# Performance work log

Measured on AMD Instinct MI355X. Metric: run time of the kernel, lower is better.

## Reference

```python
import jax, jax.numpy as jnp
import numpy as np

B, S, D, H = 2, 2048, 1024, 16
DEPTH = D // H


def setup_inputs() -> dict:
    key = jax.random.key(0)
    ks = jax.random.split(key, 12)
    inp = {
        "q": jax.random.normal(ks[0], (B, S, D), jnp.float32),
        "k": jax.random.normal(ks[1], (B, S, D), jnp.float32),
        "v": jax.random.normal(ks[2], (B, S - 1, D), jnp.float32),
        # causal mask for the sliced (S-1, S-1) score grid: 1 where masked out
        "mask": jnp.broadcast_to(
            jnp.triu(jnp.ones((S - 1, S - 1), jnp.float32), k=1), (B, S - 1, S - 1)
        ),
        "Wq": jax.random.normal(ks[3], (D, D), jnp.float32) * 0.02,
        "bq": jnp.zeros((D,), jnp.float32),
        "Wk": jax.random.normal(ks[4], (D, D), jnp.float32) * 0.02,
        "bk": jnp.zeros((D,), jnp.float32),
        "Wv": jax.random.normal(ks[5], (D, D), jnp.float32) * 0.02,
        "bv": jnp.zeros((D,), jnp.float32),
        "Wo": jax.random.normal(ks[6], (D, D), jnp.float32) * 0.02,
        "bo": jnp.zeros((D,), jnp.float32),
    }
    return inp


def _split_heads(x):
    # (B, L, D) -> (B, H, L, depth)
    b, l, _ = x.shape
    return x.reshape(b, l, H, DEPTH).transpose(0, 2, 1, 3)


def reference(q, k, v, mask, Wq, bq, Wk, bk, Wv, bv, Wo, bo):
    qq = q @ Wq + bq            # q_layers[0]
    kk = k @ Wk + bk            # k_layers[0]
    vv = v @ Wv + bv            # wv
    qh, kh, vh = _split_heads(qq), _split_heads(kk), _split_heads(vv)
    # scores: (B, H, S, S) then sliced to (B, H, S-1, S-1) as in the source
    scores = jnp.einsum('bhqd,bhkd->bhqk', qh, kh)[:, :, 1:, :-1]
    scale = 1.0 / jnp.sqrt(jnp.asarray(DEPTH, jnp.float32))
    # original casts to fp64 here; JAX default x64-disabled => computed in fp32
    logits = scores * scale + mask[:, None, :, :] * (-1e9)
    att = jax.nn.softmax(logits, axis=-1)   # (B, H, S-1, S-1)
    ctx = jnp.einsum('bhqk,bhkd->bhqd', att, vh)  # v seq len is S-1
    ctx = ctx.transpose(0, 2, 1, 3).reshape(q.shape[0], -1, D)
    out = ctx @ Wo + bo
    return out, att
```

## Files before the change

### kernel.cpp

```cpp
#include <hip/hip_runtime.h>


typedef __attribute__((ext_vector_type(8))) short bf16x8;
typedef __attribute__((ext_vector_type(4))) float f32x4;

#define MFMA_BF16(A, B, C) __builtin_amdgcn_mfma_f32_16x16x32_bf16(A, B, C, 0, 0, 0)

__device__ __forceinline__ short f2bf(float x) {
    unsigned u = __float_as_uint(x);
    u = u + 0x7FFFu + ((u >> 16) & 1u);
    return (short)(u >> 16);
}
__device__ __forceinline__ float bf2f(short s) {
    return __uint_as_float(((unsigned)(unsigned short)s) << 16);
}
__device__ __forceinline__ int imin(int a, int b) { return a < b ? a : b; }

__device__ __forceinline__ float fexp2(float x) {
#if __has_builtin(__builtin_amdgcn_exp2f)
    return __builtin_amdgcn_exp2f(x);
#else
    return __expf(x * 0.69314718055994531f);
#endif
}

__device__ __forceinline__ void dma16(const short* g, short* l) {
    __builtin_amdgcn_global_load_lds(
        (const __attribute__((address_space(1))) unsigned int*)g,
        (__attribute__((address_space(3))) unsigned int*)l, 16, 0, 0);
}

__global__ __launch_bounds__(256) void transpose_split_kernel(
    const float* __restrict__ W, short* __restrict__ Thi, short* __restrict__ Tlo) {
    __shared__ float tile[32][33];
    const int tx = threadIdx.x & 31, ty = threadIdx.x >> 5;
    const int k0 = blockIdx.x * 32, n0 = blockIdx.y * 32;
#pragma unroll
    for (int p = 0; p < 4; ++p)
        tile[ty + p * 8][tx] = W[(size_t)(k0 + ty + p * 8) * 1024 + n0 + tx];
    __syncthreads();
#pragma unroll
    for (int p = 0; p < 4; ++p) {
        int n = n0 + ty + p * 8, k = k0 + tx;
        float x = tile[tx][ty + p * 8];
        short h = f2bf(x);
        Thi[(size_t)n * 1024 + k] = h;
        if (Tlo) Tlo[(size_t)n * 1024 + k] = f2bf(x - bf2f(h));
    }
}

__global__ __launch_bounds__(256) void split_kernel(
    const float* __restrict__ X, short* __restrict__ Hi, short* __restrict__ Lo, int n8) {
    int idx = blockIdx.x * 256 + threadIdx.x;
    if (idx >= n8) return;
    float4 x0 = *((const float4*)X + (size_t)idx * 2);
    float4 x1 = *((const float4*)X + (size_t)idx * 2 + 1);
    float xs[8] = {x0.x, x0.y, x0.z, x0.w, x1.x, x1.y, x1.z, x1.w};
    bf16x8 hv, lv;
#pragma unroll
    for (int e = 0; e < 8; ++e) {
        short h = f2bf(xs[e]);
        hv[e] = h;
        lv[e] = f2bf(xs[e] - bf2f(h));
    }
    *(bf16x8*)&Hi[(size_t)idx * 8] = hv;
    if (Lo) *(bf16x8*)&Lo[(size_t)idx * 8] = lv;
}

__global__ __launch_bounds__(256) void gemm_qkv(
    const short* __restrict__ Qhi, const short* __restrict__ Qlo,
    const short* __restrict__ Khi, const short* __restrict__ Klo,
    const short* __restrict__ Vbf,
    const short* __restrict__ Wqh, const short* __restrict__ Wql,
    const short* __restrict__ Wkh, const short* __restrict__ Wkl,
    const short* __restrict__ Wvh,
    const float* __restrict__ bq, const float* __restrict__ bk,
    const float* __restrict__ bv, float qscale,
    short* __restrict__ QQh, short* __restrict__ QQl,
    short* __restrict__ KKh, short* __restrict__ KKl,
    short* __restrict__ VVo) {
    __shared__ __align__(16) short Ah[512 * 8];
    __shared__ __align__(16) short Al[512 * 8];

    const int z = blockIdx.z;
    const bool split = (z < 2);
    const short* Ahg = (z == 0) ? Qhi : ((z == 1) ? Khi : Vbf);
    const short* Alg = (z == 0) ? Qlo : Klo;
    const short* Bhg = (z == 0) ? Wqh : ((z == 1) ? Wkh : Wvh);
    const short* Blg = (z == 0) ? Wql : Wkl;
    const float* bias = (z == 0) ? bq : ((z == 1) ? bk : bv);
    const float scale = (z == 0) ? qscale : 1.0f;
    const int M = (z == 2) ? 4094 : 4096;
    short* Chi = (z == 0) ? QQh : ((z == 1) ? KKh : VVo);
    short* Clo = (z == 0) ? QQl : KKl;

    const int tid = threadIdx.x;
    const int w = tid >> 6, lane = tid & 63;
    const int quad = lane >> 4, l16 = lane & 15;
    const int m0 = blockIdx.y * 128, n0 = blockIdx.x * 64;
    const int row0 = (w & 1) * 64, col0 = (w >> 1) * 32;

    f32x4 acc[4][2];
#pragma unroll
    for (int mi = 0; mi < 4; ++mi)
#pragma unroll
        for (int ni = 0; ni < 2; ++ni) acc[mi][ni] = (f32x4){0.f, 0.f, 0.f, 0.f};

    const int a_gr = imin(m0 + (tid & 127), M - 1);

    for (int k0 = 0; k0 < 1024; k0 += 32) {
        __syncthreads();
#pragma unroll
        for (int p = 0; p < 2; ++p) {
            int idx = p * 256 + tid;
            int c = idx >> 7;
            const size_t go = (size_t)a_gr * 1024 + k0 + c * 8;
            dma16(Ahg + go, &Ah[idx * 8]);
            if (split) dma16(Alg + go, &Al[idx * 8]);
        }
        bf16x8 bfh[2], bfl[2];
#pragma unroll
        for (int ni = 0; ni < 2; ++ni) {
            const size_t bo = (size_t)(n0 + col0 + ni * 16 + l16) * 1024 + k0 + quad * 8;
            bfh[ni] = *(const bf16x8*)&Bhg[bo];
            if (split) bfl[ni] = *(const bf16x8*)&Blg[bo];
        }
        __syncthreads();

        bf16x8 af[4], afl[4];
#pragma unroll
        for (int mi = 0; mi < 4; ++mi) {
            int r = row0 + mi * 16 + l16;
            af[mi] = *(const bf16x8*)&Ah[(quad * 128 + r) * 8];
            if (split) afl[mi] = *(const bf16x8*)&Al[(quad * 128 + r) * 8];
        }
#pragma unroll
        for (int mi = 0; mi < 4; ++mi)
#pragma unroll
            for (int ni = 0; ni < 2; ++ni) {
                acc[mi][ni] = MFMA_BF16(af[mi], bfh[ni], acc[mi][ni]);
                if (split) {
                    acc[mi][ni] = MFMA_BF16(af[mi], bfl[ni], acc[mi][ni]);
                    acc[mi][ni] = MFMA_BF16(afl[mi], bfh[ni], acc[mi][ni]);
                }
            }
    }

#pragma unroll
    for (int ni = 0; ni < 2; ++ni) {
        int col = n0 + col0 + ni * 16 + l16;
        float bv_ = bias[col];
#pragma unroll
        for (int mi = 0; mi < 4; ++mi) {
#pragma unroll
            for (int r = 0; r < 4; ++r) {
                int row = m0 + row0 + mi * 16 + quad * 4 + r;
                if (row < M) {
                    float c = (acc[mi][ni][r] + bv_) * scale;
                    size_t off = (size_t)row * 1024 + col;
                    short hsv = f2bf(c);
                    Chi[off] = hsv;
                    if (split) Clo[off] = f2bf(c - bf2f(hsv));
                }
            }
        }
    }
}

__global__ __launch_bounds__(256) void gemm_o(
    const short* __restrict__ Ahg, int M, const short* __restrict__ Bhg,
    const float* __restrict__ bias, float* __restrict__ Cf) {
    __shared__ __align__(16) short Ah[512 * 8];

    const int tid = threadIdx.x;
    const int w = tid >> 6, lane = tid & 63;
    const int quad = lane >> 4, l16 = lane & 15;
    const int m0 = blockIdx.y * 128, n0 = blockIdx.x * 64;
    const int row0 = (w & 1) * 64, col0 = (w >> 1) * 32;

    f32x4 acc[4][2];
#pragma unroll
    for (int mi = 0; mi < 4; ++mi)
#pragma unroll
        for (int ni = 0; ni < 2; ++ni) acc[mi][ni] = (f32x4){0.f, 0.f, 0.f, 0.f};

    const int a_gr = imin(m0 + (tid & 127), M - 1);

    for (int k0 = 0; k0 < 1024; k0 += 32) {
        __syncthreads();
#pragma unroll
        for (int p = 0; p < 2; ++p) {
            int idx = p * 256 + tid;
            int c = idx >> 7;
            dma16(Ahg + (size_t)a_gr * 1024 + k0 + c * 8, &Ah[idx * 8]);
        }
        bf16x8 bfh[2];
#pragma unroll
        for (int ni = 0; ni < 2; ++ni) {
            const size_t bo = (size_t)(n0 + col0 + ni * 16 + l16) * 1024 + k0 + quad * 8;
            bfh[ni] = *(const bf16x8*)&Bhg[bo];
        }
        __syncthreads();

        bf16x8 af[4];
#pragma unroll
        for (int mi = 0; mi < 4; ++mi)
            af[mi] = *(const bf16x8*)&Ah[(quad * 128 + row0 + mi * 16 + l16) * 8];
#pragma unroll
        for (int mi = 0; mi < 4; ++mi)
#pragma unroll
            for (int ni = 0; ni < 2; ++ni)
                acc[mi][ni] = MFMA_BF16(af[mi], bfh[ni], acc[mi][ni]);
    }

#pragma unroll
    for (int ni = 0; ni < 2; ++ni) {
        int col = n0 + col0 + ni * 16 + l16;
        float bv_ = bias[col];
#pragma unroll
        for (int mi = 0; mi < 4; ++mi)
#pragma unroll
            for (int r = 0; r < 4; ++r) {
                int row = m0 + row0 + mi * 16 + quad * 4 + r;
                if (row < M) Cf[(size_t)row * 1024 + col] = acc[mi][ni][r] + bv_;
            }
    }
}

__global__ __launch_bounds__(256) void transpose_v_kernel(
    const short* __restrict__ VV, short* __restrict__ VT) {
    __shared__ short t[64][72];
    const int tid = threadIdx.x;
    const int st = blockIdx.x & 31, bh = blockIdx.x >> 5;
    const int b = bh >> 4, h = bh & 15;
    const int s0 = st * 64;
    {
        int seq = s0 + (tid >> 2), d0 = (tid & 3) * 16;
        int seqc = imin(seq, 2046);
        const short* src = VV + ((size_t)(b * 2047 + seqc)) * 1024 + h * 64 + d0;
        bf16x8 v0 = *(const bf16x8*)src;
        bf16x8 v1 = *(const bf16x8*)(src + 8);
        bool ok = (seq <= 2046);
#pragma unroll
        for (int e = 0; e < 8; ++e) {
            t[d0 + e][tid >> 2] = ok ? v0[e] : (short)0;
            t[d0 + 8 + e][tid >> 2] = ok ? v1[e] : (short)0;
        }
    }
    __syncthreads();
    {
        int d = tid >> 2, sc2 = (tid & 3) * 16;
        bf16x8 o0, o1;
#pragma unroll
        for (int e = 0; e < 8; ++e) {
            o0[e] = t[d][sc2 + e];
            o1[e] = t[d][sc2 + 8 + e];
        }
        short* dst = VT + ((size_t)(bh * 64 + d)) * 2048 + s0 + sc2;
        *(bf16x8*)dst = o0;
        *(bf16x8*)(dst + 8) = o1;
    }
}

__global__ __launch_bounds__(512) void attn_kernel(
    const short* __restrict__ QQh, const short* __restrict__ QQl,
    const short* __restrict__ KKh, const short* __restrict__ KKl,
    const short* __restrict__ VT,
    float* __restrict__ att, short* __restrict__ CTX) {
    __shared__ __align__(16) short Kh[512 * 8];
    __shared__ __align__(16) short Kl[512 * 8];
    __shared__ __align__(16) short Vt[512 * 8];
    __shared__ __align__(16) short Ps[8][16 * 72];

    const int tid = threadIdx.x;
    const int w = tid >> 6, lane = tid & 63;
    const int quad = lane >> 4, l16 = lane & 15;
    const int bx = blockIdx.x;
    const int qt = 15 - (bx >> 5);
    const int bh = bx & 31;
    const int h = bh & 15, b = bh >> 4;
    const int i0 = qt * 128;

    const int i_frag = i0 + w * 16 + l16;
    const int qrow = imin(i_frag + 1, 2047);
    const size_t qoff = ((size_t)(b * 2048 + qrow)) * 1024 + h * 64;
    const bf16x8 qh0 = *(const bf16x8*)&QQh[qoff + 0 + quad * 8];
    const bf16x8 qh1 = *(const bf16x8*)&QQh[qoff + 32 + quad * 8];
    const bf16x8 ql0 = *(const bf16x8*)&QQl[qoff + 0 + quad * 8];
    const bf16x8 ql1 = *(const bf16x8*)&QQl[qoff + 32 + quad * 8];

    const int i_max = imin(i0 + 127, 2046);
    const int jt_max = i_max >> 6;
    const int wave_imax = imin(i0 + w * 16 + 15, 2046);
    const int rowbase = i0 + w * 16 + quad * 4;

    const int dk = tid & 63;
    const int dc = tid >> 6;

    float lsum[4] = {0.f, 0.f, 0.f, 0.f};

    auto stA = [&](int jt, short* dst) {
        dma16(KKh + ((size_t)(b * 2048 + jt * 64 + dk)) * 1024 + h * 64 + dc * 8,
              &dst[tid * 8]);
    };
    stA(0, Kh);
    __syncthreads();
    int cur = 0;
    for (int jt = 0; jt <= jt_max; ++jt) {
        if (jt < jt_max) stA(jt + 1, cur ? Kh : Kl);
        if (jt * 64 <= wave_imax) {
            const short* Kc = cur ? Kl : Kh;
#pragma unroll
            for (int s = 0; s < 4; ++s) {
                f32x4 sc = (f32x4){0.f, 0.f, 0.f, 0.f};
#pragma unroll
                for (int c = 0; c < 2; ++c) {
                    bf16x8 kh = *(const bf16x8*)&Kc[((c * 4 + quad) * 64 + s * 16 + l16) * 8];
                    sc = MFMA_BF16(c ? qh1 : qh0, kh, sc);
                    sc = MFMA_BF16(c ? ql1 : ql0, kh, sc);
                }
                int j = jt * 64 + s * 16 + l16;
#pragma unroll
                for (int r = 0; r < 4; ++r) {
                    int i = rowbase + r;
                    if (j <= i && i <= 2046) lsum[r] += fexp2(sc[r]);
                }
            }
        }
        __syncthreads();
        cur ^= 1;
    }
#pragma unroll
    for (int m = 1; m < 16; m <<= 1) {
#pragma unroll
        for (int r = 0; r < 4; ++r) lsum[r] += __shfl_xor(lsum[r], m, 64);
    }
    float linv[4];
#pragma unroll
    for (int r = 0; r < 4; ++r) linv[r] = 1.0f / lsum[r];

    f32x4 cacc[4];
#pragma unroll
    for (int t = 0; t < 4; ++t) cacc[t] = (f32x4){0.f, 0.f, 0.f, 0.f};

    for (int jt = 0; jt <= jt_max; ++jt) {
        const int j0 = jt * 64;
        __syncthreads();
        {
            const size_t ko = ((size_t)(b * 2048 + j0 + dk)) * 1024 + h * 64 + dc * 8;
            dma16(KKh + ko, &Kh[tid * 8]);
            dma16(KKl + ko, &Kl[tid * 8]);
            dma16(VT + ((size_t)(bh * 64 + dk)) * 2048 + j0 + dc * 8, &Vt[tid * 8]);
        }
        __syncthreads();
        if (j0 <= wave_imax) {
#pragma unroll
            for (int s = 0; s < 4; ++s) {
                f32x4 sc = (f32x4){0.f, 0.f, 0.f, 0.f};
#pragma unroll
                for (int c = 0; c < 2; ++c) {
                    const int ci = ((c * 4 + quad) * 64 + s * 16 + l16) * 8;
                    bf16x8 kh = *(const bf16x8*)&Kh[ci];
                    bf16x8 kl = *(const bf16x8*)&Kl[ci];
                    bf16x8 ah = c ? qh1 : qh0;
                    bf16x8 al = c ? ql1 : ql0;
                    sc = MFMA_BF16(ah, kh, sc);
                    sc = MFMA_BF16(ah, kl, sc);
                    sc = MFMA_BF16(al, kh, sc);
                }
                int j = j0 + s * 16 + l16;
#pragma unroll
                for (int r = 0; r < 4; ++r) {
                    int i = rowbase + r;
                    bool valid = (j <= i) && (i <= 2046);
                    float p = valid ? fexp2(sc[r]) * linv[r] : 0.0f;
                    if (i <= 2046 && j <= 2046)
                        att[((size_t)bh * 2047 + i) * 2047 + j] = p;
                    Ps[w][(quad * 4 + r) * 72 + s * 16 + l16] = f2bf(p);
                }
            }
#pragma unroll
            for (int c = 0; c < 2; ++c) {
                bf16x8 pa = *(const bf16x8*)&Ps[w][l16 * 72 + c * 32 + quad * 8];
#pragma unroll
                for (int t = 0; t < 4; ++t) {
                    bf16x8 vb = *(const bf16x8*)&Vt[((c * 4 + quad) * 64 + t * 16 + l16) * 8];
                    cacc[t] = MFMA_BF16(pa, vb, cacc[t]);
                }
            }
        } else {
#pragma unroll
            for (int s = 0; s < 4; ++s) {
                int j = j0 + s * 16 + l16;
#pragma unroll
                for (int r = 0; r < 4; ++r) {
                    int i = rowbase + r;
                    if (i <= 2046 && j <= 2046)
                        att[((size_t)bh * 2047 + i) * 2047 + j] = 0.0f;
                }
            }
        }
    }

#pragma unroll
    for (int t = 0; t < 4; ++t) {
#pragma unroll
        for (int r = 0; r < 4; ++r) {
            int i = rowbase + r;
            if (i <= 2046)
                CTX[((size_t)(b * 2047 + i)) * 1024 + h * 64 + t * 16 + l16] = f2bf(cacc[t][r]);
        }
    }

    const int js = (jt_max + 1) * 64;
    if (js < 2047) {
        const float4 z4 = {0.f, 0.f, 0.f, 0.f};
        for (int i = i0; i <= i_max; ++i) {
            const size_t base = (size_t)(bh * 2047 + i) * 2047;
            float* rowp = att + base;
            int aligned = js + (int)((4 - ((base + js) & 3)) & 3);
            if (aligned > 2047) aligned = 2047;
            for (int c = js + tid; c < aligned; c += 512) rowp[c] = 0.0f;
            int nv = (2047 - aligned) >> 2;
            for (int q = tid; q < nv; q += 512)
                *(float4*)(rowp + aligned + q * 4) = z4;
            for (int c = aligned + nv * 4 + tid; c < 2047; c += 512) rowp[c] = 0.0f;
        }
    }
}

extern "C" void kernel_launch(void* const* d_in, const int* in_sizes, int n_in,
                              void* d_out, int out_size, void* d_ws, size_t ws_size,
                              hipStream_t stream) {
    (void)in_sizes; (void)n_in; (void)out_size; (void)ws_size;
    const float* q  = (const float*)d_in[0];
    const float* k  = (const float*)d_in[1];
    const float* v  = (const float*)d_in[2];
    const float* Wq = (const float*)d_in[4];
    const float* bq = (const float*)d_in[5];
    const float* Wk = (const float*)d_in[6];
    const float* bk = (const float*)d_in[7];
    const float* Wv = (const float*)d_in[8];
    const float* bv = (const float*)d_in[9];
    const float* Wo = (const float*)d_in[10];
    const float* bo = (const float*)d_in[11];

    float* out = (float*)d_out;
    float* att = out + (size_t)2 * 2047 * 1024;

    char* ws = (char*)d_ws;
    size_t off = 0;
    auto alloc = [&](size_t bytes) -> void* {
        void* p = ws + off;
        off += (bytes + 255) & ~(size_t)255;
        return p;
    };
    short* Wqt_h = (short*)alloc((size_t)1024 * 1024 * 2);
    short* Wqt_l = (short*)alloc((size_t)1024 * 1024 * 2);
    short* Wkt_h = (short*)alloc((size_t)1024 * 1024 * 2);
    short* Wkt_l = (short*)alloc((size_t)1024 * 1024 * 2);
    short* Wvt_h = (short*)alloc((size_t)1024 * 1024 * 2);
    short* Wot_h = (short*)alloc((size_t)1024 * 1024 * 2);
    short* Qhi = (short*)alloc((size_t)4096 * 1024 * 2);
    short* Qlo = (short*)alloc((size_t)4096 * 1024 * 2);
    short* Khi = (short*)alloc((size_t)4096 * 1024 * 2);
    short* Klo = (short*)alloc((size_t)4096 * 1024 * 2);
    short* Vbf = (short*)alloc((size_t)4096 * 1024 * 2);
    short* QQh = (short*)alloc((size_t)4096 * 1024 * 2);
    short* QQl = (short*)alloc((size_t)4096 * 1024 * 2);
    short* KKh = (short*)alloc((size_t)4096 * 1024 * 2);
    short* KKl = (short*)alloc((size_t)4096 * 1024 * 2);
    short* VV  = (short*)alloc((size_t)4096 * 1024 * 2);
    short* VT  = (short*)alloc((size_t)2048 * 2048 * 2 * 2);
    short* CTX = (short*)alloc((size_t)4096 * 1024 * 2);

    dim3 tgrid(32, 32);
    transpose_split_kernel<<<tgrid, 256, 0, stream>>>(Wq, Wqt_h, Wqt_l);
    transpose_split_kernel<<<tgrid, 256, 0, stream>>>(Wk, Wkt_h, Wkt_l);
    transpose_split_kernel<<<tgrid, 256, 0, stream>>>(Wv, Wvt_h, nullptr);
    transpose_split_kernel<<<tgrid, 256, 0, stream>>>(Wo, Wot_h, nullptr);

    split_kernel<<<2048, 256, 0, stream>>>(q, Qhi, Qlo, 4096 * 1024 / 8);
    split_kernel<<<2048, 256, 0, stream>>>(k, Khi, Klo, 4096 * 1024 / 8);
    split_kernel<<<2047, 256, 0, stream>>>(v, Vbf, nullptr, 4094 * 1024 / 8);

    const float qscale = 0.125f * 1.44269504088896341f;
    gemm_qkv<<<dim3(16, 32, 3), 256, 0, stream>>>(
        Qhi, Qlo, Khi, Klo, Vbf, Wqt_h, Wqt_l, Wkt_h, Wkt_l, Wvt_h,
        bq, bk, bv, qscale, QQh, QQl, KKh, KKl, VV);

    transpose_v_kernel<<<dim3(32 * 32), 256, 0, stream>>>(VV, VT);

    attn_kernel<<<dim3(16 * 32), 512, 0, stream>>>(QQh, QQl, KKh, KKl, VT, att, CTX);

    gemm_o<<<dim3(16, 32), 256, 0, stream>>>(CTX, 4094, Wot_h, bo, out);
}
```

Before: 1.002 ms.

## Widen GEMM tiles to 128x128 with LDS-staged B, merge prep kernel launches

```diff
diff --git a/kernel.cpp b/kernel.cpp
--- a/kernel.cpp
+++ b/kernel.cpp
@@ -30,8 +30,17 @@
         (__attribute__((address_space(3))) unsigned int*)l, 16, 0, 0);
 }
 
-__global__ __launch_bounds__(256) void transpose_split_kernel(
-    const float* __restrict__ W, short* __restrict__ Thi, short* __restrict__ Tlo) {
+__global__ __launch_bounds__(256) void transpose_split4(
+    const float* __restrict__ Wq, const float* __restrict__ Wk,
+    const float* __restrict__ Wv, const float* __restrict__ Wo,
+    short* __restrict__ Tqh, short* __restrict__ Tql,
+    short* __restrict__ Tkh, short* __restrict__ Tkl,
+    short* __restrict__ Tvh, short* __restrict__ Toh) {
+    const int z = blockIdx.z;
+    const float* W = (z == 0) ? Wq : (z == 1) ? Wk : (z == 2) ? Wv : Wo;
+    short* Thi = (z == 0) ? Tqh : (z == 1) ? Tkh : (z == 2) ? Tvh : Toh;
+    short* Tlo = (z == 0) ? Tql : (z == 1) ? Tkl : nullptr;
+
     __shared__ float tile[32][33];
     const int tx = threadIdx.x & 31, ty = threadIdx.x >> 5;
     const int k0 = blockIdx.x * 32, n0 = blockIdx.y * 32;
@@ -49,8 +58,18 @@
     }
 }
 
-__global__ __launch_bounds__(256) void split_kernel(
-    const float* __restrict__ X, short* __restrict__ Hi, short* __restrict__ Lo, int n8) {
+__global__ __launch_bounds__(256) void split3(
+    const float* __restrict__ q, const float* __restrict__ k,
+    const float* __restrict__ v,
+    short* __restrict__ Qhi, short* __restrict__ Qlo,
+    short* __restrict__ Khi, short* __restrict__ Klo,
+    short* __restrict__ Vbf) {
+    const int z = blockIdx.z;
+    const float* X = (z == 0) ? q : (z == 1) ? k : v;
+    short* Hi = (z == 0) ? Qhi : (z == 1) ? Khi : Vbf;
+    short* Lo = (z == 0) ? Qlo : (z == 1) ? Klo : nullptr;
+    const int n8 = (z == 2) ? (4094 * 1024 / 8) : (4096 * 1024 / 8);
+
     int idx = blockIdx.x * 256 + threadIdx.x;
     if (idx >= n8) return;
     float4 x0 = *((const float4*)X + (size_t)idx * 2);
@@ -81,6 +100,8 @@
     short* __restrict__ VVo) {
     __shared__ __align__(16) short Ah[512 * 8];
     __shared__ __align__(16) short Al[512 * 8];
+    __shared__ __align__(16) short Bh[512 * 8];
+    __shared__ __align__(16) short Bl[512 * 8];
 
     const int z = blockIdx.z;
     const bool split = (z < 2);
@@ -97,68 +118,72 @@
     const int tid = threadIdx.x;
     const int w = tid >> 6, lane = tid & 63;
     const int quad = lane >> 4, l16 = lane & 15;
-    const int m0 = blockIdx.y * 128, n0 = blockIdx.x * 64;
-    const int row0 = (w & 1) * 64, col0 = (w >> 1) * 32;
-
-    f32x4 acc[4][2];
+    const int m0 = blockIdx.y * 128, n0 = blockIdx.x * 128;
+    const int wr = (w & 1) * 64, wc = (w >> 1) * 64;
+
+    f32x4 acc[4][4];
 #pragma unroll
     for (int mi = 0; mi < 4; ++mi)
 #pragma unroll
-        for (int ni = 0; ni < 2; ++ni) acc[mi][ni] = (f32x4){0.f, 0.f, 0.f, 0.f};
+        for (int ni = 0; ni < 4; ++ni) acc[mi][ni] = (f32x4){0.f, 0.f, 0.f, 0.f};
 
     const int a_gr = imin(m0 + (tid & 127), M - 1);
+    const int b_gr = n0 + (tid & 127);
 
     for (int k0 = 0; k0 < 1024; k0 += 32) {
         __syncthreads();
 #pragma unroll
         for (int p = 0; p < 2; ++p) {
-            int idx = p * 256 + tid;
-            int c = idx >> 7;
-            const size_t go = (size_t)a_gr * 1024 + k0 + c * 8;
-            dma16(Ahg + go, &Ah[idx * 8]);
-            if (split) dma16(Alg + go, &Al[idx * 8]);
-        }
-        bf16x8 bfh[2], bfl[2];
-#pragma unroll
-        for (int ni = 0; ni < 2; ++ni) {
-            const size_t bo = (size_t)(n0 + col0 + ni * 16 + l16) * 1024 + k0 + quad * 8;
-            bfh[ni] = *(const bf16x8*)&Bhg[bo];
-            if (split) bfl[ni] = *(const bf16x8*)&Blg[bo];
+            const int idx = p * 256 + tid;
+            const size_t ga = (size_t)a_gr * 1024 + k0 + (idx >> 7) * 8;
+            const size_t gb = (size_t)b_gr * 1024 + k0 + (idx >> 7) * 8;
+            dma16(Ahg + ga, &Ah[idx * 8]);
+            dma16(Bhg + gb, &Bh[idx * 8]);
+            if (split) {
+                dma16(Alg + ga, &Al[idx * 8]);
+                dma16(Blg + gb, &Bl[idx * 8]);
+            }
         }
         __syncthreads();
 
         bf16x8 af[4], afl[4];
 #pragma unroll
         for (int mi = 0; mi < 4; ++mi) {
-            int r = row0 + mi * 16 + l16;
+            const int r = wr + mi * 16 + l16;
             af[mi] = *(const bf16x8*)&Ah[(quad * 128 + r) * 8];
             if (split) afl[mi] = *(const bf16x8*)&Al[(quad * 128 + r) * 8];
         }
 #pragma unroll
-        for (int mi = 0; mi < 4; ++mi)
-#pragma unroll
-            for (int ni = 0; ni < 2; ++ni) {
-                acc[mi][ni] = MFMA_BF16(af[mi], bfh[ni], acc[mi][ni]);
-                if (split) {
-                    acc[mi][ni] = MFMA_BF16(af[mi], bfl[ni], acc[mi][ni]);
-                    acc[mi][ni] = MFMA_BF16(afl[mi], bfh[ni], acc[mi][ni]);
-                }
-            }
-    }
-
-#pragma unroll
-    for (int ni = 0; ni < 2; ++ni) {
-        int col = n0 + col0 + ni * 16 + l16;
-        float bv_ = bias[col];
+        for (int ni = 0; ni < 4; ++ni) {
+            const int cdx = wc + ni * 16 + l16;
+            const bf16x8 bfh = *(const bf16x8*)&Bh[(quad * 128 + cdx) * 8];
+#pragma unroll
+            for (int mi = 0; mi < 4; ++mi)
+                acc[mi][ni] = MFMA_BF16(af[mi], bfh, acc[mi][ni]);
+            if (split) {
+                const bf16x8 bfl = *(const bf16x8*)&Bl[(quad * 128 + cdx) * 8];
+#pragma unroll
+                for (int mi = 0; mi < 4; ++mi) {
+                    acc[mi][ni] = MFMA_BF16(af[mi], bfl, acc[mi][ni]);
+                    acc[mi][ni] = MFMA_BF16(afl[mi], bfh, acc[mi][ni]);
+                }
+            }
+        }
+    }
+
+#pragma unroll
+    for (int ni = 0; ni < 4; ++ni) {
+        const int col = n0 + wc + ni * 16 + l16;
+        const float bv_ = bias[col];
 #pragma unroll
         for (int mi = 0; mi < 4; ++mi) {
 #pragma unroll
             for (int r = 0; r < 4; ++r) {
-                int row = m0 + row0 + mi * 16 + quad * 4 + r;
+                const int row = m0 + wr + mi * 16 + quad * 4 + r;
                 if (row < M) {
-                    float c = (acc[mi][ni][r] + bv_) * scale;
-                    size_t off = (size_t)row * 1024 + col;
-                    short hsv = f2bf(c);
+                    const float c = (acc[mi][ni][r] + bv_) * scale;
+                    const size_t off = (size_t)row * 1024 + col;
+                    const short hsv = f2bf(c);
                     Chi[off] = hsv;
                     if (split) Clo[off] = f2bf(c - bf2f(hsv));
                 }
@@ -171,57 +196,55 @@
     const short* __restrict__ Ahg, int M, const short* __restrict__ Bhg,
     const float* __restrict__ bias, float* __restrict__ Cf) {
     __shared__ __align__(16) short Ah[512 * 8];
+    __shared__ __align__(16) short Bh[512 * 8];
 
     const int tid = threadIdx.x;
     const int w = tid >> 6, lane = tid & 63;
     const int quad = lane >> 4, l16 = lane & 15;
-    const int m0 = blockIdx.y * 128, n0 = blockIdx.x * 64;
-    const int row0 = (w & 1) * 64, col0 = (w >> 1) * 32;
-
-    f32x4 acc[4][2];
+    const int m0 = blockIdx.y * 128, n0 = blockIdx.x * 128;
+    const int wr = (w & 1) * 64, wc = (w >> 1) * 64;
+
+    f32x4 acc[4][4];
 #pragma unroll
     for (int mi = 0; mi < 4; ++mi)
 #pragma unroll
-        for (int ni = 0; ni < 2; ++ni) acc[mi][ni] = (f32x4){0.f, 0.f, 0.f, 0.f};
+        for (int ni = 0; ni < 4; ++ni) acc[mi][ni] = (f32x4){0.f, 0.f, 0.f, 0.f};
 
     const int a_gr = imin(m0 + (tid & 127), M - 1);
+    const int b_gr = n0 + (tid & 127);
 
     for (int k0 = 0; k0 < 1024; k0 += 32) {
         __syncthreads();
 #pragma unroll
         for (int p = 0; p < 2; ++p) {
-            int idx = p * 256 + tid;
-            int c = idx >> 7;
-            dma16(Ahg + (size_t)a_gr * 1024 + k0 + c * 8, &Ah[idx * 8]);
-        }
-        bf16x8 bfh[2];
-#pragma unroll
-        for (int ni = 0; ni < 2; ++ni) {
-            const size_t bo = (size_t)(n0 + col0 + ni * 16 + l16) * 1024 + k0 + quad * 8;
-            bfh[ni] = *(const bf16x8*)&Bhg[bo];
+            const int idx = p * 256 + tid;
+            dma16(Ahg + (size_t)a_gr * 1024 + k0 + (idx >> 7) * 8, &Ah[idx * 8]);
+            dma16(Bhg + (size_t)b_gr * 1024 + k0 + (idx >> 7) * 8, &Bh[idx * 8]);
         }
         __syncthreads();
 
         bf16x8 af[4];
 #pragma unroll
         for (int mi = 0; mi < 4; ++mi)
-            af[mi] = *(const bf16x8*)&Ah[(quad * 128 + row0 + mi * 16 + l16) * 8];
+            af[mi] = *(const bf16x8*)&Ah[(quad * 128 + wr + mi * 16 + l16) * 8];
+#pragma unroll
+        for (int ni = 0; ni < 4; ++ni) {
+            const bf16x8 bfh = *(const bf16x8*)&Bh[(quad * 128 + wc + ni * 16 + l16) * 8];
+#pragma unroll
+            for (int mi = 0; mi < 4; ++mi)
+                acc[mi][ni] = MFMA_BF16(af[mi], bfh, acc[mi][ni]);
+        }
+    }
+
+#pragma unroll
+    for (int ni = 0; ni < 4; ++ni) {
+        const int col = n0 + wc + ni * 16 + l16;
+        const float bv_ = bias[col];
 #pragma unroll
         for (int mi = 0; mi < 4; ++mi)
 #pragma unroll
-            for (int ni = 0; ni < 2; ++ni)
-                acc[mi][ni] = MFMA_BF16(af[mi], bfh[ni], acc[mi][ni]);
-    }
-
-#pragma unroll
-    for (int ni = 0; ni < 2; ++ni) {
-        int col = n0 + col0 + ni * 16 + l16;
-        float bv_ = bias[col];
-#pragma unroll
-        for (int mi = 0; mi < 4; ++mi)
-#pragma unroll
             for (int r = 0; r < 4; ++r) {
-                int row = m0 + row0 + mi * 16 + quad * 4 + r;
+                const int row = m0 + wr + mi * 16 + quad * 4 + r;
                 if (row < M) Cf[(size_t)row * 1024 + col] = acc[mi][ni][r] + bv_;
             }
     }
@@ -474,18 +497,14 @@
     short* VT  = (short*)alloc((size_t)2048 * 2048 * 2 * 2);
     short* CTX = (short*)alloc((size_t)4096 * 1024 * 2);
 
-    dim3 tgrid(32, 32);
-    transpose_split_kernel<<<tgrid, 256, 0, stream>>>(Wq, Wqt_h, Wqt_l);
-    transpose_split_kernel<<<tgrid, 256, 0, stream>>>(Wk, Wkt_h, Wkt_l);
-    transpose_split_kernel<<<tgrid, 256, 0, stream>>>(Wv, Wvt_h, nullptr);
-    transpose_split_kernel<<<tgrid, 256, 0, stream>>>(Wo, Wot_h, nullptr);
-
-    split_kernel<<<2048, 256, 0, stream>>>(q, Qhi, Qlo, 4096 * 1024 / 8);
-    split_kernel<<<2048, 256, 0, stream>>>(k, Khi, Klo, 4096 * 1024 / 8);
-    split_kernel<<<2047, 256, 0, stream>>>(v, Vbf, nullptr, 4094 * 1024 / 8);
+    transpose_split4<<<dim3(32, 32, 4), 256, 0, stream>>>(
+        Wq, Wk, Wv, Wo, Wqt_h, Wqt_l, Wkt_h, Wkt_l, Wvt_h, Wot_h);
+
+    split3<<<dim3(2048, 1, 3), 256, 0, stream>>>(
+        q, k, v, Qhi, Qlo, Khi, Klo, Vbf);
 
     const float qscale = 0.125f * 1.44269504088896341f;
-    gemm_qkv<<<dim3(16, 32, 3), 256, 0, stream>>>(
+    gemm_qkv<<<dim3(8, 32, 3), 256, 0, stream>>>(
         Qhi, Qlo, Khi, Klo, Vbf, Wqt_h, Wqt_l, Wkt_h, Wkt_l, Wvt_h,
         bq, bk, bv, qscale, QQh, QQl, KKh, KKl, VV);
 
@@ -493,5 +512,5 @@
 
     attn_kernel<<<dim3(16 * 32), 512, 0, stream>>>(QQh, QQl, KKh, KKl, VT, att, CTX);
 
-    gemm_o<<<dim3(16, 32), 256, 0, stream>>>(CTX, 4094, Wot_h, bo, out);
-}
+    gemm_o<<<dim3(8, 32), 256, 0, stream>>>(CTX, 4094, Wot_h, bo, out);
+}
```

Result: faster. 959.8 us (-4.2%).
